# Kernel tuning notes

Hardware: AMD Instinct MI355X
Metric: run time of the kernel (lower is better)

The kernel has to match this reference:

```python
import jax, jax.numpy as jnp
import numpy as np

B, C = 32768, 1024
T = 2.0  # softmax temperature


def setup_inputs() -> dict:
    key = jax.random.key(0)
    k1, k2, k3, k4 = jax.random.split(key, 4)
    outputs = jax.random.normal(k1, (B, C), dtype=jnp.float32)
    # targets in [0, C-2] so that target+1 is a valid class (as the torch code requires)
    targets = jax.random.randint(k2, (B,), 0, C - 1, dtype=jnp.int32)
    ages = jax.random.randint(k3, (B,), 0, 100, dtype=jnp.int32)
    weight = jax.random.uniform(k4, (C,), dtype=jnp.float32)
    return {"outputs": outputs, "targets": targets, "ages": ages, "weight": weight}


def reference(outputs, targets, ages, weight):
    # outputs: (B, C) logits; targets: (B,) int; ages: (B,) int; weight: (C,)
    Cn = outputs.shape[-1]
    agef = ages.astype(outputs.dtype)
    # vectorized version of the per-row python loop: rows with 50 < age < 60
    # move (age-50)*0.1 probability mass from class t to class t+1
    in_band = jnp.logical_and(agef > 50.0, agef < 60.0)
    delta = jnp.where(in_band, (agef - 50.0) * 0.1, 0.0)  # (B,)
    oh = jax.nn.one_hot(targets, Cn, dtype=outputs.dtype)  # (B, C)
    oh_next = jax.nn.one_hot(targets + 1, Cn, dtype=outputs.dtype)
    soft_targets = oh * (1.0 - delta[:, None]) + oh_next * delta[:, None]
    logp = jax.nn.log_softmax(outputs / T, axis=-1)  # (B, C)
    per_row = jnp.sum(-soft_targets * logp * weight[None, :], axis=1)  # (B,)
    return jnp.mean(per_row)
```

## Files before the change

### kernel.cpp

```cpp
#include <hip/hip_runtime.h>
#include <hip/hip_bf16.h>
#include <math.h>

#define BB 32768
#define CC 1024
#define INV_T 0.5f
#define ROWS_PER_BLOCK 8
#define NBLOCKS (BB / ROWS_PER_BLOCK)

typedef float floatx4 __attribute__((ext_vector_type(4)));

__global__ __launch_bounds__(512) void row_loss_kernel(
    const float* __restrict__ outputs,
    const int* __restrict__ targets,
    const int* __restrict__ ages,
    const float* __restrict__ weight,
    float* __restrict__ partial)
{
    const int wave = threadIdx.x >> 6;
    const int lane = threadIdx.x & 63;
    const int row  = blockIdx.x * ROWS_PER_BLOCK + wave;

    const float* rowp = outputs + (size_t)row * CC;
    const floatx4* rp4 = (const floatx4*)rowp;

    floatx4 v[4];
#pragma unroll
    for (int k = 0; k < 4; ++k)
        v[k] = __builtin_nontemporal_load(&rp4[k * 64 + lane]);

    float s = 0.0f;
#pragma unroll
    for (int k = 0; k < 4; ++k) {
        s += __expf(v[k].x * INV_T);
        s += __expf(v[k].y * INV_T);
        s += __expf(v[k].z * INV_T);
        s += __expf(v[k].w * INV_T);
    }
#pragma unroll
    for (int mask = 32; mask >= 1; mask >>= 1)
        s += __shfl_xor(s, mask, 64);

    __shared__ float wave_loss[ROWS_PER_BLOCK];

    if (lane == 0) {
        const float lse = __logf(s);
        const int   t    = targets[row];
        const float agef = (float)ages[row];
        const float delta = (agef > 50.0f && agef < 60.0f) ? (agef - 50.0f) * 0.1f : 0.0f;
        const float y_t  = rowp[t]     * INV_T;
        const float y_t1 = rowp[t + 1] * INV_T;
        const float loss = -((1.0f - delta) * (y_t  - lse) * weight[t]
                           +          delta * (y_t1 - lse) * weight[t + 1]);
        wave_loss[wave] = loss;
    }
    __syncthreads();
    if (threadIdx.x == 0) {
        float b = 0.0f;
#pragma unroll
        for (int w = 0; w < ROWS_PER_BLOCK; ++w) b += wave_loss[w];
        partial[blockIdx.x] = b;
    }
}

__global__ __launch_bounds__(256) void final_reduce_kernel(
    const float* __restrict__ partial, float* __restrict__ out)
{
    float s = 0.0f;
#pragma unroll
    for (int i = 0; i < NBLOCKS / 256; ++i)
        s += partial[i * 256 + threadIdx.x];

#pragma unroll
    for (int mask = 32; mask >= 1; mask >>= 1)
        s += __shfl_xor(s, mask, 64);

    __shared__ float ws[4];
    const int wave = threadIdx.x >> 6;
    const int lane = threadIdx.x & 63;
    if (lane == 0) ws[wave] = s;
    __syncthreads();
    if (threadIdx.x == 0) {
        float tot = ws[0] + ws[1] + ws[2] + ws[3];
        out[0] = tot / (float)BB;
    }
}

extern "C" void kernel_launch(void* const* d_in, const int* in_sizes, int n_in,
                              void* d_out, int out_size, void* d_ws, size_t ws_size,
                              hipStream_t stream) {
    const float* outputs = (const float*)d_in[0];
    const int*   targets = (const int*)d_in[1];
    const int*   ages    = (const int*)d_in[2];
    const float* weight  = (const float*)d_in[3];
    float* out = (float*)d_out;
    float* partial = (float*)d_ws;

    row_loss_kernel<<<NBLOCKS, 512, 0, stream>>>(outputs, targets, ages, weight, partial);
    final_reduce_kernel<<<1, 256, 0, stream>>>(partial, out);
}
```

Measured before the change: 186.1 us.

## Process two rows per wave and drop block-level shared reduction

Each wave now handles two rows, issuing all eight 16-byte loads for both rows before computing, which doubles memory-level parallelism per wave. The per-block shared-memory reduction and __syncthreads are removed: each wave writes its own partial, so the final reduce sums four times as many partials, using four independent accumulators. The risks are higher register pressure per wave and a slightly longer single-block final reduction.

```diff
diff --git a/kernel.cpp b/kernel.cpp
--- a/kernel.cpp
+++ b/kernel.cpp
@@ -5,8 +5,11 @@
 #define BB 32768
 #define CC 1024
 #define INV_T 0.5f
-#define ROWS_PER_BLOCK 8
+#define WAVES_PER_BLOCK 8
+#define ROWS_PER_WAVE 2
+#define ROWS_PER_BLOCK (WAVES_PER_BLOCK * ROWS_PER_WAVE)
 #define NBLOCKS (BB / ROWS_PER_BLOCK)
+#define NPART (BB / ROWS_PER_WAVE)
 
 typedef float floatx4 __attribute__((ext_vector_type(4)));
 
@@ -17,59 +20,71 @@
     const float* __restrict__ weight,
     float* __restrict__ partial)
 {
-    const int wave = threadIdx.x >> 6;
-    const int lane = threadIdx.x & 63;
-    const int row  = blockIdx.x * ROWS_PER_BLOCK + wave;
+    const int wave  = threadIdx.x >> 6;
+    const int lane  = threadIdx.x & 63;
+    const int gwave = blockIdx.x * WAVES_PER_BLOCK + wave;
+    const int row0  = gwave * ROWS_PER_WAVE;
 
-    const float* rowp = outputs + (size_t)row * CC;
-    const floatx4* rp4 = (const floatx4*)rowp;
+    const float* rowpA = outputs + (size_t)row0 * CC;
+    const float* rowpB = rowpA + CC;
+    const floatx4* rpA = (const floatx4*)rowpA;
+    const floatx4* rpB = (const floatx4*)rowpB;
 
-    floatx4 v[4];
-#pragma unroll
-    for (int k = 0; k < 4; ++k)
-        v[k] = __builtin_nontemporal_load(&rp4[k * 64 + lane]);
-
-    float s = 0.0f;
+    floatx4 a[4], b[4];
 #pragma unroll
     for (int k = 0; k < 4; ++k) {
-        s += __expf(v[k].x * INV_T);
-        s += __expf(v[k].y * INV_T);
-        s += __expf(v[k].z * INV_T);
-        s += __expf(v[k].w * INV_T);
+        a[k] = __builtin_nontemporal_load(&rpA[k * 64 + lane]);
+        b[k] = __builtin_nontemporal_load(&rpB[k * 64 + lane]);
     }
+
+    float pa[4], pb[4];
 #pragma unroll
-    for (int mask = 32; mask >= 1; mask >>= 1)
-        s += __shfl_xor(s, mask, 64);
+    for (int k = 0; k < 4; ++k) {
+        pa[k] = __expf(a[k].x * INV_T) + __expf(a[k].y * INV_T)
+              + __expf(a[k].z * INV_T) + __expf(a[k].w * INV_T);
+        pb[k] = __expf(b[k].x * INV_T) + __expf(b[k].y * INV_T)
+              + __expf(b[k].z * INV_T) + __expf(b[k].w * INV_T);
+    }
+    float sa = (pa[0] + pa[1]) + (pa[2] + pa[3]);
+    float sb = (pb[0] + pb[1]) + (pb[2] + pb[3]);
 
-    __shared__ float wave_loss[ROWS_PER_BLOCK];
+#pragma unroll
+    for (int mask = 32; mask >= 1; mask >>= 1) {
+        sa += __shfl_xor(sa, mask, 64);
+        sb += __shfl_xor(sb, mask, 64);
+    }
 
     if (lane == 0) {
-        const float lse = __logf(s);
-        const int   t    = targets[row];
-        const float agef = (float)ages[row];
-        const float delta = (agef > 50.0f && agef < 60.0f) ? (agef - 50.0f) * 0.1f : 0.0f;
-        const float y_t  = rowp[t]     * INV_T;
-        const float y_t1 = rowp[t + 1] * INV_T;
-        const float loss = -((1.0f - delta) * (y_t  - lse) * weight[t]
-                           +          delta * (y_t1 - lse) * weight[t + 1]);
-        wave_loss[wave] = loss;
-    }
-    __syncthreads();
-    if (threadIdx.x == 0) {
-        float b = 0.0f;
-#pragma unroll
-        for (int w = 0; w < ROWS_PER_BLOCK; ++w) b += wave_loss[w];
-        partial[blockIdx.x] = b;
+        const float lseA = __logf(sa);
+        const float lseB = __logf(sb);
+
+        const int   tA    = targets[row0];
+        const int   tB    = targets[row0 + 1];
+        const float ageA  = (float)ages[row0];
+        const float ageB  = (float)ages[row0 + 1];
+        const float dA = (ageA > 50.0f && ageA < 60.0f) ? (ageA - 50.0f) * 0.1f : 0.0f;
+        const float dB = (ageB > 50.0f && ageB < 60.0f) ? (ageB - 50.0f) * 0.1f : 0.0f;
+
+        const float lossA = -((1.0f - dA) * (rowpA[tA]     * INV_T - lseA) * weight[tA]
+                            +          dA * (rowpA[tA + 1] * INV_T - lseA) * weight[tA + 1]);
+        const float lossB = -((1.0f - dB) * (rowpB[tB]     * INV_T - lseB) * weight[tB]
+                            +          dB * (rowpB[tB + 1] * INV_T - lseB) * weight[tB + 1]);
+        partial[gwave] = lossA + lossB;
     }
 }
 
 __global__ __launch_bounds__(256) void final_reduce_kernel(
     const float* __restrict__ partial, float* __restrict__ out)
 {
-    float s = 0.0f;
+    float s0 = 0.0f, s1 = 0.0f, s2 = 0.0f, s3 = 0.0f;
 #pragma unroll
-    for (int i = 0; i < NBLOCKS / 256; ++i)
-        s += partial[i * 256 + threadIdx.x];
+    for (int i = 0; i < NPART / (256 * 4); ++i) {
+        s0 += partial[(i * 4 + 0) * 256 + threadIdx.x];
+        s1 += partial[(i * 4 + 1) * 256 + threadIdx.x];
+        s2 += partial[(i * 4 + 2) * 256 + threadIdx.x];
+        s3 += partial[(i * 4 + 3) * 256 + threadIdx.x];
+    }
+    float s = (s0 + s1) + (s2 + s3);
 
 #pragma unroll
     for (int mask = 32; mask >= 1; mask >>= 1)
```

Result: no change. 188.7 us (+1.4%).
